# Performance work log

Measured on AMD Instinct MI355X. Metric: run time of the kernel, lower is better.

The kernel has to match this reference:

```python
import jax, jax.numpy as jnp
import numpy as np

N_SEQ, BS, E, H = 2048, 8, 512, 8
HD = E // H  # 64


def setup_inputs() -> dict:
    key = jax.random.key(0)
    k1, k2, k3 = jax.random.split(key, 3)
    seq = jax.random.normal(k1, (N_SEQ, BS, E), dtype=jnp.float32)
    # xavier_uniform for Linear(E, 3E): bound = sqrt(6/(fan_in+fan_out))
    b_qkv_w = float(np.sqrt(6.0 / (E + 3 * E)))
    W_qkv = jax.random.uniform(k2, (3 * E, E), minval=-b_qkv_w, maxval=b_qkv_w, dtype=jnp.float32)
    b_out_w = float(np.sqrt(6.0 / (E + E)))
    W_out = jax.random.uniform(k3, (E, E), minval=-b_out_w, maxval=b_out_w, dtype=jnp.float32)
    b_qkv = jnp.zeros((3 * E,), dtype=jnp.float32)
    b_out = jnp.zeros((E,), dtype=jnp.float32)
    return {"seq": seq, "W_qkv": W_qkv, "b_qkv": b_qkv, "W_out": W_out, "b_out": b_out}


def reference(seq, W_qkv, b_qkv, W_out, b_out):
    n, bs, e = seq.shape
    # fused QKV projection: [n, bs, 3E]
    qkv = jnp.einsum('nbe,fe->nbf', seq, W_qkv) + b_qkv
    # [n, bs, 3, H, HD] -> q/k/v each [n, bs*H, HD] (bs outer, H inner)
    qkv = qkv.reshape(n, bs, 3, H, HD)
    q = qkv[:, :, 0].reshape(n, bs * H, HD)
    k = qkv[:, :, 1].reshape(n, bs * H, HD)
    v = qkv[:, :, 2].reshape(n, bs * H, HD)
    scale = 1.0 / jnp.sqrt(jnp.asarray(HD, dtype=seq.dtype))
    # full [bs*H, n, n] score matrix as in the original
    attn = jnp.einsum('qbd,kbd->bqk', q * scale, k)
    attn = jax.nn.softmax(attn, axis=-1)
    out = jnp.einsum('bqk,kbd->qbd', attn, v)  # [n, bs*H, HD]
    out = out.reshape(n, bs, e)
    return jnp.einsum('nbe,fe->nbf', out, W_out) + b_out
```

## Files before the change

### kernel.cpp

```cpp
#include <hip/hip_runtime.h>
#include <stdint.h>

typedef unsigned short ushort_t;
typedef unsigned int uint32;
typedef __attribute__((ext_vector_type(8))) short short8;
typedef __attribute__((ext_vector_type(4))) float f32x4;
typedef __attribute__((ext_vector_type(16))) float f32x16;
typedef __attribute__((ext_vector_type(4))) uint32 uint4v;

#define NSEQ 2048
#define BSZ 8
#define EMB 512
#define NHEAD 8
#define HDIM 64
#define MTOK (NSEQ*BSZ)
#define NH_TOT (BSZ*NHEAD)
#define NP (NSEQ/128)

#define VMCNT0 asm volatile("s_waitcnt vmcnt(0)" ::: "memory")
#define BAR __builtin_amdgcn_s_barrier()

__device__ __forceinline__ ushort_t f2bf(float f) {
  uint32_t u = __builtin_bit_cast(uint32_t, f);
  u += 0x7FFFu + ((u >> 16) & 1u);
  return (ushort_t)(u >> 16);
}
__device__ __forceinline__ float bf2f(ushort_t u) {
  uint32_t x = ((uint32_t)u) << 16;
  return __builtin_bit_cast(float, x);
}

__device__ __forceinline__ void gll16(const void* g, void* l) {
  __builtin_amdgcn_global_load_lds(
      (const __attribute__((address_space(1))) void*)g,
      (__attribute__((address_space(3))) void*)l, 16, 0, 0);
}

__device__ __forceinline__ int SW(int r) { return (r & 7) ^ ((r >> 3) & 7); }

__global__ void cvt3(const float* __restrict__ a, ushort_t* __restrict__ oa, int na4,
                     const float* __restrict__ b, ushort_t* __restrict__ ob, int nb4,
                     const float* __restrict__ c, ushort_t* __restrict__ oc, int nc4) {
  int i = blockIdx.x * blockDim.x + threadIdx.x;
  const float* src; ushort_t* dst; int j = i;
  if (j < na4) { src = a; dst = oa; }
  else {
    j -= na4;
    if (j < nb4) { src = b; dst = ob; }
    else { j -= nb4; if (j >= nc4) return; src = c; dst = oc; }
  }
  float4 v = reinterpret_cast<const float4*>(src)[j];
  union { ushort_t u[4]; uint64_t q; } o;
  o.u[0] = f2bf(v.x); o.u[1] = f2bf(v.y); o.u[2] = f2bf(v.z); o.u[3] = f2bf(v.w);
  reinterpret_cast<uint64_t*>(dst)[j] = o.q;
}

template<int MODE>
__global__ __launch_bounds__(256) void gemm_bt(
    const ushort_t* __restrict__ A, const ushort_t* __restrict__ B,
    const float* __restrict__ bias,
    float* __restrict__ Cf, ushort_t* __restrict__ Cq,
    int M, int N, int K)
{
  __shared__ __align__(16) ushort_t As[128*64];
  __shared__ __align__(16) ushort_t Bs[128*64];
  const int t = threadIdx.x;
  const int w = t >> 6, l = t & 63;

  const int nbx = gridDim.x;
  const int bid = blockIdx.x + nbx * blockIdx.y;
  const int per = (nbx * gridDim.y) >> 3;
  const int swz = (bid & 7) * per + (bid >> 3);
  const int tm = (swz / nbx) * 128, tn = (swz % nbx) * 128;
  const int wm = w >> 1, wn = w & 1;

  f32x4 acc[4][4] = {};

  for (int k0 = 0; k0 < K; k0 += 64) {
    #pragma unroll
    for (int j = 0; j < 4; ++j) {
      int row = j*32 + w*8 + (l >> 3);
      int cole = ((l & 7) * 8) ^ ((row & 7) << 3);
      const ushort_t* ga = A + (size_t)(tm + row) * K + k0 + cole;
      const ushort_t* gb = B + (size_t)(tn + row) * K + k0 + cole;
      gll16(ga, As + j*2048 + w*512 + l*8);
      gll16(gb, Bs + j*2048 + w*512 + l*8);
    }
    __syncthreads();
    #pragma unroll
    for (int kk = 0; kk < 2; ++kk) {
      short8 af[4], bfr[4];
      #pragma unroll
      for (int mi = 0; mi < 4; ++mi) {
        int row = wm*64 + mi*16 + (l & 15);
        int byte = row*128 + ((kk*64 + ((l >> 4) * 16)) ^ ((row & 7) << 4));
        af[mi] = *reinterpret_cast<const short8*>(reinterpret_cast<const char*>(As) + byte);
      }
      #pragma unroll
      for (int ni = 0; ni < 4; ++ni) {
        int row = wn*64 + ni*16 + (l & 15);
        int byte = row*128 + ((kk*64 + ((l >> 4) * 16)) ^ ((row & 7) << 4));
        bfr[ni] = *reinterpret_cast<const short8*>(reinterpret_cast<const char*>(Bs) + byte);
      }
      #pragma unroll
      for (int mi = 0; mi < 4; ++mi)
        #pragma unroll
        for (int ni = 0; ni < 4; ++ni)
          acc[mi][ni] = __builtin_amdgcn_mfma_f32_16x16x32_bf16(af[mi], bfr[ni], acc[mi][ni], 0, 0, 0);
    }
    __syncthreads();
  }

  #pragma unroll
  for (int mi = 0; mi < 4; ++mi) {
    #pragma unroll
    for (int ni = 0; ni < 4; ++ni) {
      #pragma unroll
      for (int r = 0; r < 4; ++r) {
        int row = tm + wm*64 + mi*16 + ((l >> 4) * 4) + r;
        int col = tn + wn*64 + ni*16 + (l & 15);
        float v = acc[mi][ni][r] + bias[col];
        if constexpr (MODE == 1) {
          Cf[(size_t)row * N + col] = v;
        } else {
          int w3 = col >> 9, hx = (col >> 6) & 7, hd = col & 63;
          int n = row >> 3, bb = row & 7;
          Cq[(size_t)w3 * ((size_t)NH_TOT * NSEQ * HDIM)
             + ((size_t)(bb * NHEAD + hx) * NSEQ + n) * HDIM + hd] = f2bf(v);
        }
      }
    }
  }
}

__global__ __launch_bounds__(256) void transpose_v(
    const ushort_t* __restrict__ V, ushort_t* __restrict__ VT)
{
  __shared__ __align__(16) ushort_t T[64*64];
  const int t = threadIdx.x;
  const int head = blockIdx.y;
  const int n0 = blockIdx.x * 64;
  const size_t base = (size_t)head * NSEQ * HDIM;
  const int r = t >> 3, c0 = (t & 7) * 8;

  short8 a = *reinterpret_cast<const short8*>(V + base + (size_t)(n0 + r) * HDIM + c0);
  short8 b = *reinterpret_cast<const short8*>(V + base + (size_t)(n0 + r + 32) * HDIM + c0);
  #pragma unroll
  for (int e = 0; e < 8; ++e) {
    int d = c0 + e; int sw = SW(d) << 4;
    *reinterpret_cast<ushort_t*>(reinterpret_cast<char*>(T) + d*128 + ((r*2) ^ sw)) = (ushort_t)a[e];
    *reinterpret_cast<ushort_t*>(reinterpret_cast<char*>(T) + d*128 + (((r+32)*2) ^ sw)) = (ushort_t)b[e];
  }
  __syncthreads();
  #pragma unroll
  for (int i = 0; i < 2; ++i) {
    int d = (t >> 3) + 32*i, ch = t & 7;
    short8 v = *reinterpret_cast<const short8*>(
        reinterpret_cast<const char*>(T) + d*128 + ((ch*16) ^ (SW(d) << 4)));
    *reinterpret_cast<short8*>(VT + (size_t)head * HDIM * NSEQ + (size_t)d * NSEQ + n0 + ch*8) = v;
  }
}

#define CSC 0.18033688011112042f

__global__ __launch_bounds__(256, 2) void attn_fwd(
    const ushort_t* __restrict__ Qb, const ushort_t* __restrict__ Kb,
    const ushort_t* __restrict__ VTb, ushort_t* __restrict__ Ob)
{
  __shared__ __align__(16) ushort_t Ks[2][2][64*64];
  __shared__ __align__(16) ushort_t Vs[2][2][64*64];
  const int t = threadIdx.x, w = t >> 6, l = t & 63;
  const int lq = l & 31, h = l >> 5;
  const int L = blockIdx.x + 8 * blockIdx.y;
  const int Tid = (L & 7) * 64 + (L >> 3);
  const int bh = Tid >> 3, qt = Tid & 7;
  const int b = bh >> 3, hh = bh & 7;
  const size_t hbase  = (size_t)bh * NSEQ * HDIM;
  const size_t vtbase = (size_t)bh * HDIM * NSEQ;
  const int qbase = qt*256 + w*64;

  short8 qreg[2][4];
  #pragma unroll
  for (int qb = 0; qb < 2; ++qb)
    #pragma unroll
    for (int kd = 0; kd < 4; ++kd) {
      short8 raw = *reinterpret_cast<const short8*>(
          Qb + hbase + (size_t)(qbase + qb*32 + lq) * HDIM + kd*16 + h*8);
      short8 q;
      #pragma unroll
      for (int e = 0; e < 8; ++e)
        q[e] = (short)f2bf(bf2f((ushort_t)raw[e]) * CSC);
      qreg[qb][kd] = q;
    }

  f32x16 Oacc[2][2] = {};
  f32x16 lacc0 = {}, lacc1 = {};

  const short ONE = (short)0x3F80;
  short8 ones = { ONE, ONE, ONE, ONE, ONE, ONE, ONE, ONE };

  const int srow = t >> 3;
  const int scol = (t & 7) * 8;
  const int c0 = scol ^ (SW(srow) << 3);
  const int c1 = scol ^ (SW(srow + 32) << 3);
  const ushort_t* Kg0 = Kb  + hbase  + (size_t)srow       * HDIM + c0;
  const ushort_t* Kg1 = Kb  + hbase  + (size_t)(srow+32)  * HDIM + c1;
  const ushort_t* Vg0 = VTb + vtbase + (size_t)srow       * NSEQ + c0;
  const ushort_t* Vg1 = VTb + vtbase + (size_t)(srow+32)  * NSEQ + c1;

  auto STAGE = [&](int bi, int p) {
    #pragma unroll
    for (int ss = 0; ss < 2; ++ss) {
      int kt = p*2 + ss;
      size_t ko = (size_t)kt * 64 * HDIM;
      int    vo = kt * 64;
      gll16(Kg0 + ko, &Ks[bi][ss][0]    + t*8);
      gll16(Kg1 + ko, &Ks[bi][ss][2048] + t*8);
      gll16(Vg0 + vo, &Vs[bi][ss][0]    + t*8);
      gll16(Vg1 + vo, &Vs[bi][ss][2048] + t*8);
    }
  };

  VMCNT0;
  STAGE(0, 0);

  int cur = 0;
  #pragma unroll 1
  for (int p = 0; p < NP; ++p) {
    VMCNT0;
    BAR;
    if (p + 1 < NP) STAGE(cur ^ 1, p + 1);

    #pragma unroll
    for (int ss = 0; ss < 2; ++ss) {
      const char* KsC = reinterpret_cast<const char*>(&Ks[cur][ss][0]);
      const char* VsC = reinterpret_cast<const char*>(&Vs[cur][ss][0]);

      short8 kf[2][4];
      #pragma unroll
      for (int rp = 0; rp < 2; ++rp) {
        int row = rp*32 + lq;
        int swr = SW(row) << 4;
        #pragma unroll
        for (int kd = 0; kd < 4; ++kd)
          kf[rp][kd] = *reinterpret_cast<const short8*>(
              KsC + row*128 + ((kd*32 + h*16) ^ swr));
      }

      uint32 pa0[4][4], pa1[4][4];

      {
        f32x16 s0 = {}, s1 = {};
        __builtin_amdgcn_s_setprio(1);
        #pragma unroll
        for (int kd = 0; kd < 4; ++kd) {
          s0 = __builtin_amdgcn_mfma_f32_32x32x16_bf16(kf[0][kd], qreg[0][kd], s0, 0, 0, 0);
          s1 = __builtin_amdgcn_mfma_f32_32x32x16_bf16(kf[1][kd], qreg[0][kd], s1, 0, 0, 0);
        }
        __builtin_amdgcn_s_setprio(0);
        #pragma unroll
        for (int r = 0; r < 16; ++r) {
          s0[r] = __builtin_amdgcn_exp2f(s0[r]);
          s1[r] = __builtin_amdgcn_exp2f(s1[r]);
        }
        uint32 w0[8], w1[8];
        #pragma unroll
        for (int i = 0; i < 8; ++i) {
          float a0 = s0[2*i], b0 = s0[2*i+1];
          float a1 = s1[2*i], b1 = s1[2*i+1];
          asm("v_cvt_pk_bf16_f32 %0, %1, %2" : "=v"(w0[i]) : "v"(a0), "v"(b0));
          asm("v_cvt_pk_bf16_f32 %0, %1, %2" : "=v"(w1[i]) : "v"(a1), "v"(b1));
        }
        #pragma unroll
        for (int sg = 0; sg < 2; ++sg) {
          uint32 a, bb;
          a = w0[4*sg+0]; bb = w0[4*sg+2];
          asm("v_permlane32_swap_b32 %0, %1" : "+v"(a), "+v"(bb));
          pa0[sg][0] = a; pa0[sg][2] = bb;
          a = w0[4*sg+1]; bb = w0[4*sg+3];
          asm("v_permlane32_swap_b32 %0, %1" : "+v"(a), "+v"(bb));
          pa0[sg][1] = a; pa0[sg][3] = bb;
          a = w1[4*sg+0]; bb = w1[4*sg+2];
          asm("v_permlane32_swap_b32 %0, %1" : "+v"(a), "+v"(bb));
          pa0[2+sg][0] = a; pa0[2+sg][2] = bb;
          a = w1[4*sg+1]; bb = w1[4*sg+3];
          asm("v_permlane32_swap_b32 %0, %1" : "+v"(a), "+v"(bb));
          pa0[2+sg][1] = a; pa0[2+sg][3] = bb;
        }
      }

      {
        f32x16 s0 = {}, s1 = {};
        __builtin_amdgcn_s_setprio(1);
        #pragma unroll
        for (int kd = 0; kd < 4; ++kd) {
          s0 = __builtin_amdgcn_mfma_f32_32x32x16_bf16(kf[0][kd], qreg[1][kd], s0, 0, 0, 0);
          s1 = __builtin_amdgcn_mfma_f32_32x32x16_bf16(kf[1][kd], qreg[1][kd], s1, 0, 0, 0);
        }
        __builtin_amdgcn_s_setprio(0);
        #pragma unroll
        for (int r = 0; r < 16; ++r) {
          s0[r] = __builtin_amdgcn_exp2f(s0[r]);
          s1[r] = __builtin_amdgcn_exp2f(s1[r]);
        }
        uint32 w0[8], w1[8];
        #pragma unroll
        for (int i = 0; i < 8; ++i) {
          float a0 = s0[2*i], b0 = s0[2*i+1];
          float a1 = s1[2*i], b1 = s1[2*i+1];
          asm("v_cvt_pk_bf16_f32 %0, %1, %2" : "=v"(w0[i]) : "v"(a0), "v"(b0));
          asm("v_cvt_pk_bf16_f32 %0, %1, %2" : "=v"(w1[i]) : "v"(a1), "v"(b1));
        }
        #pragma unroll
        for (int sg = 0; sg < 2; ++sg) {
          uint32 a, bb;
          a = w0[4*sg+0]; bb = w0[4*sg+2];
          asm("v_permlane32_swap_b32 %0, %1" : "+v"(a), "+v"(bb));
          pa1[sg][0] = a; pa1[sg][2] = bb;
          a = w0[4*sg+1]; bb = w0[4*sg+3];
          asm("v_permlane32_swap_b32 %0, %1" : "+v"(a), "+v"(bb));
          pa1[sg][1] = a; pa1[sg][3] = bb;
          a = w1[4*sg+0]; bb = w1[4*sg+2];
          asm("v_permlane32_swap_b32 %0, %1" : "+v"(a), "+v"(bb));
          pa1[2+sg][0] = a; pa1[2+sg][2] = bb;
          a = w1[4*sg+1]; bb = w1[4*sg+3];
          asm("v_permlane32_swap_b32 %0, %1" : "+v"(a), "+v"(bb));
          pa1[2+sg][1] = a; pa1[2+sg][3] = bb;
        }
      }

      short8 vf[2][4];
      #pragma unroll
      for (int dt = 0; dt < 2; ++dt) {
        int d = dt*32 + lq;
        int swd = SW(d) << 4;
        #pragma unroll
        for (int km = 0; km < 4; ++km)
          vf[dt][km] = *reinterpret_cast<const short8*>(
              VsC + d*128 + ((km*32 + h*16) ^ swd));
      }

      __builtin_amdgcn_s_setprio(1);
      #pragma unroll
      for (int km = 0; km < 4; ++km) {
        uint4v u0; u0[0] = pa0[km][0]; u0[1] = pa0[km][1]; u0[2] = pa0[km][2]; u0[3] = pa0[km][3];
        short8 paf0 = __builtin_bit_cast(short8, u0);
        uint4v u1; u1[0] = pa1[km][0]; u1[1] = pa1[km][1]; u1[2] = pa1[km][2]; u1[3] = pa1[km][3];
        short8 paf1 = __builtin_bit_cast(short8, u1);
        Oacc[0][0] = __builtin_amdgcn_mfma_f32_32x32x16_bf16(paf0, vf[0][km], Oacc[0][0], 0, 0, 0);
        lacc0      = __builtin_amdgcn_mfma_f32_32x32x16_bf16(paf0, ones,     lacc0,      0, 0, 0);
        Oacc[0][1] = __builtin_amdgcn_mfma_f32_32x32x16_bf16(paf0, vf[1][km], Oacc[0][1], 0, 0, 0);
        Oacc[1][0] = __builtin_amdgcn_mfma_f32_32x32x16_bf16(paf1, vf[0][km], Oacc[1][0], 0, 0, 0);
        lacc1      = __builtin_amdgcn_mfma_f32_32x32x16_bf16(paf1, ones,     lacc1,      0, 0, 0);
        Oacc[1][1] = __builtin_amdgcn_mfma_f32_32x32x16_bf16(paf1, vf[1][km], Oacc[1][1], 0, 0, 0);
      }
      __builtin_amdgcn_s_setprio(0);
    }

    cur ^= 1;
  }

  #pragma unroll
  for (int r = 0; r < 16; ++r) {
    int qrow = (r & 3) + 8*(r >> 2) + 4*h;
    float li0 = __builtin_amdgcn_rcpf(lacc0[r]);
    float li1 = __builtin_amdgcn_rcpf(lacc1[r]);
    #pragma unroll
    for (int dt = 0; dt < 2; ++dt) {
      int d = dt*32 + lq;
      int n0 = qbase + qrow;
      int n1 = qbase + 32 + qrow;
      Ob[((size_t)n0 * BSZ + b) * EMB + hh*64 + d] = f2bf(Oacc[0][dt][r] * li0);
      Ob[((size_t)n1 * BSZ + b) * EMB + hh*64 + d] = f2bf(Oacc[1][dt][r] * li1);
    }
  }
}

extern "C" void kernel_launch(void* const* d_in, const int* in_sizes, int n_in,
                              void* d_out, int out_size, void* d_ws, size_t ws_size,
                              hipStream_t stream) {
  (void)in_sizes; (void)n_in; (void)out_size; (void)ws_size;
  const float* seq  = (const float*)d_in[0];
  const float* Wqkv = (const float*)d_in[1];
  const float* bqkv = (const float*)d_in[2];
  const float* Wout = (const float*)d_in[3];
  const float* bout = (const float*)d_in[4];
  float* out = (float*)d_out;

  ushort_t* seq_bf  = (ushort_t*)d_ws;
  ushort_t* wqkv_bf = seq_bf  + (size_t)MTOK * EMB;
  ushort_t* wout_bf = wqkv_bf + (size_t)3 * EMB * EMB;
  ushort_t* qkvbuf  = wout_bf + (size_t)EMB * EMB;
  ushort_t* vtbuf   = qkvbuf  + (size_t)3 * NH_TOT * NSEQ * HDIM;
  ushort_t* attno   = qkvbuf  + (size_t)2 * NH_TOT * NSEQ * HDIM;

  const int na4 = MTOK*EMB/4, nb4 = 3*EMB*EMB/4, nc4 = EMB*EMB/4;
  cvt3<<<(na4+nb4+nc4 + 255)/256, 256, 0, stream>>>(
      seq, seq_bf, na4, Wqkv, wqkv_bf, nb4, Wout, wout_bf, nc4);

  gemm_bt<0><<<dim3(12, 128), 256, 0, stream>>>(seq_bf, wqkv_bf, bqkv, nullptr, qkvbuf,
                                                MTOK, 3*EMB, EMB);

  const ushort_t* Qb  = qkvbuf;
  const ushort_t* Kb  = qkvbuf + (size_t)NH_TOT * NSEQ * HDIM;
  const ushort_t* Vb  = Kb     + (size_t)NH_TOT * NSEQ * HDIM;

  transpose_v<<<dim3(32, 64), 256, 0, stream>>>(Vb, vtbuf);

  attn_fwd<<<dim3(8, 64), 256, 0, stream>>>(Qb, Kb, vtbuf, attno);

  gemm_bt<1><<<dim3(4, 128), 256, 0, stream>>>(attno, wout_bf, bout, out, nullptr,
                                               MTOK, EMB, EMB);
}
```

Baseline: 154.0 us.

## Fuse V transpose into QKV GEMM epilogue via shared-memory staging

```diff
diff --git a/kernel.cpp b/kernel.cpp
--- a/kernel.cpp
+++ b/kernel.cpp
@@ -59,11 +59,12 @@
 __global__ __launch_bounds__(256) void gemm_bt(
     const ushort_t* __restrict__ A, const ushort_t* __restrict__ B,
     const float* __restrict__ bias,
-    float* __restrict__ Cf, ushort_t* __restrict__ Cq,
+    float* __restrict__ Cf, ushort_t* __restrict__ Cq, ushort_t* __restrict__ VTq,
     int M, int N, int K)
 {
-  __shared__ __align__(16) ushort_t As[128*64];
-  __shared__ __align__(16) ushort_t Bs[128*64];
+  __shared__ __align__(16) ushort_t SH[2][128*64];
+  ushort_t* As = &SH[0][0];
+  ushort_t* Bs = &SH[1][0];
   const int t = threadIdx.x;
   const int w = t >> 6, l = t & 63;
 
@@ -109,6 +110,43 @@
           acc[mi][ni] = __builtin_amdgcn_mfma_f32_16x16x32_bf16(af[mi], bfr[ni], acc[mi][ni], 0, 0, 0);
     }
     __syncthreads();
+  }
+
+  if (MODE == 0 && tn >= 2*EMB) {
+    ushort_t* T = &SH[0][0];
+    #pragma unroll
+    for (int mi = 0; mi < 4; ++mi) {
+      #pragma unroll
+      for (int ni = 0; ni < 4; ++ni) {
+        #pragma unroll
+        for (int r = 0; r < 4; ++r) {
+          int rowl = wm*64 + mi*16 + ((l >> 4) * 4) + r;
+          int coll = wn*64 + ni*16 + (l & 15);
+          float v = acc[mi][ni][r] + bias[tn + coll];
+          int b = rowl & 7, nloc = rowl >> 3;
+          int hx = coll >> 6, hd = coll & 63;
+          int rowT = (hx*8 + b)*64 + hd;
+          int pc = (nloc >> 3) ^ (rowT & 1);
+          T[rowT*16 + pc*8 + (nloc & 7)] = f2bf(v);
+        }
+      }
+    }
+    __syncthreads();
+    const int hxg0 = (tn >> 6) & 7;
+    #pragma unroll
+    for (int i = 0; i < 8; ++i) {
+      int c = i*256 + t;
+      int rowT = c >> 1, lc = c & 1;
+      int pc = lc ^ (rowT & 1);
+      short8 val = *reinterpret_cast<const short8*>(&T[rowT*16 + pc*8]);
+      int hx = rowT >> 9;
+      int b  = (rowT >> 6) & 7;
+      int hd = rowT & 63;
+      int head = b*NHEAD + hxg0 + hx;
+      size_t n = (size_t)(tm >> 3) + lc*8;
+      *reinterpret_cast<short8*>(VTq + (size_t)head * HDIM * NSEQ + (size_t)hd * NSEQ + n) = val;
+    }
+    return;
   }
 
   #pragma unroll
@@ -130,34 +168,6 @@
         }
       }
     }
-  }
-}
-
-__global__ __launch_bounds__(256) void transpose_v(
-    const ushort_t* __restrict__ V, ushort_t* __restrict__ VT)
-{
-  __shared__ __align__(16) ushort_t T[64*64];
-  const int t = threadIdx.x;
-  const int head = blockIdx.y;
-  const int n0 = blockIdx.x * 64;
-  const size_t base = (size_t)head * NSEQ * HDIM;
-  const int r = t >> 3, c0 = (t & 7) * 8;
-
-  short8 a = *reinterpret_cast<const short8*>(V + base + (size_t)(n0 + r) * HDIM + c0);
-  short8 b = *reinterpret_cast<const short8*>(V + base + (size_t)(n0 + r + 32) * HDIM + c0);
-  #pragma unroll
-  for (int e = 0; e < 8; ++e) {
-    int d = c0 + e; int sw = SW(d) << 4;
-    *reinterpret_cast<ushort_t*>(reinterpret_cast<char*>(T) + d*128 + ((r*2) ^ sw)) = (ushort_t)a[e];
-    *reinterpret_cast<ushort_t*>(reinterpret_cast<char*>(T) + d*128 + (((r+32)*2) ^ sw)) = (ushort_t)b[e];
-  }
-  __syncthreads();
-  #pragma unroll
-  for (int i = 0; i < 2; ++i) {
-    int d = (t >> 3) + 32*i, ch = t & 7;
-    short8 v = *reinterpret_cast<const short8*>(
-        reinterpret_cast<const char*>(T) + d*128 + ((ch*16) ^ (SW(d) << 4)));
-    *reinterpret_cast<short8*>(VT + (size_t)head * HDIM * NSEQ + (size_t)d * NSEQ + n0 + ch*8) = v;
   }
 }
 
@@ -399,16 +409,13 @@
       seq, seq_bf, na4, Wqkv, wqkv_bf, nb4, Wout, wout_bf, nc4);
 
   gemm_bt<0><<<dim3(12, 128), 256, 0, stream>>>(seq_bf, wqkv_bf, bqkv, nullptr, qkvbuf,
-                                                MTOK, 3*EMB, EMB);
+                                                vtbuf, MTOK, 3*EMB, EMB);
 
   const ushort_t* Qb  = qkvbuf;
   const ushort_t* Kb  = qkvbuf + (size_t)NH_TOT * NSEQ * HDIM;
-  const ushort_t* Vb  = Kb     + (size_t)NH_TOT * NSEQ * HDIM;
-
-  transpose_v<<<dim3(32, 64), 256, 0, stream>>>(Vb, vtbuf);
 
   attn_fwd<<<dim3(8, 64), 256, 0, stream>>>(Qb, Kb, vtbuf, attno);
 
   gemm_bt<1><<<dim3(4, 128), 256, 0, stream>>>(attno, wout_bf, bout, out, nullptr,
-                                               MTOK, EMB, EMB);
-}
+                                               nullptr, MTOK, EMB, EMB);
+}
```

After: 153.0 us. No clear change (-0.6%).
